# Kernel tuning notes

Hardware: AMD Instinct MI355X
Metric: run time of the kernel (lower is better)

## Reference

```python
import jax, jax.numpy as jnp
import numpy as np

N = 200000   # nodes (Elliptic-scale)
E = 500000   # directed edges
F = 166      # in_channels / node feature dim
H = 128      # hidden_channels
C = 2        # out_channels
T = 49       # number of time steps


def setup_inputs() -> dict:
    key = jax.random.key(0)
    ks = jax.random.split(key, 12)
    x = jax.random.normal(ks[0], (N, F), jnp.float32)
    edge_index = jax.random.randint(ks[1], (2, E), 0, N, dtype=jnp.int32)
    time_step = jax.random.randint(ks[2], (N,), 0, T, dtype=jnp.int32)
    sF = 1.0 / np.sqrt(F)
    sH = 1.0 / np.sqrt(H)
    initial_w = jax.random.uniform(ks[3], (F, F), jnp.float32, -sF, sF)
    gru_w_ih = jax.random.uniform(ks[4], (3 * F, F), jnp.float32, -sF, sF)
    gru_w_hh = jax.random.uniform(ks[5], (3 * F, F), jnp.float32, -sF, sF)
    gru_b_ih = jax.random.uniform(ks[6], (3 * F,), jnp.float32, -sF, sF)
    gru_b_hh = jax.random.uniform(ks[7], (3 * F,), jnp.float32, -sF, sF)
    proj_w = jax.random.uniform(ks[8], (H, F), jnp.float32, -sF, sF)
    proj_b = jax.random.uniform(ks[9], (H,), jnp.float32, -sF, sF)
    cls_w = jax.random.uniform(ks[10], (C, H), jnp.float32, -sH, sH)
    cls_b = jax.random.uniform(ks[11], (C,), jnp.float32, -sH, sH)
    return {"x": x, "edge_index": edge_index, "time_step": time_step,
            "initial_w": initial_w, "gru_w_ih": gru_w_ih, "gru_w_hh": gru_w_hh,
            "gru_b_ih": gru_b_ih, "gru_b_hh": gru_b_hh,
            "proj_w": proj_w, "proj_b": proj_b, "cls_w": cls_w, "cls_b": cls_b}


def reference(x, edge_index, time_step, initial_w, gru_w_ih, gru_w_hh,
              gru_b_ih, gru_b_hh, proj_w, proj_b, cls_w, cls_b):
    src, dst = edge_index[0], edge_index[1]
    n = x.shape[0]

    def gru(W):
        # torch.nn.GRU single step, input = hidden = W  (FxF matrix, rows = batch)
        gi = W @ gru_w_ih.T + gru_b_ih
        gh = W @ gru_w_hh.T + gru_b_hh
        i_r, i_z, i_n = jnp.split(gi, 3, axis=-1)
        h_r, h_z, h_n = jnp.split(gh, 3, axis=-1)
        r = jax.nn.sigmoid(i_r + h_r)
        z = jax.nn.sigmoid(i_z + h_z)
        nn_ = jnp.tanh(i_n + r * h_n)
        return (1.0 - z) * nn_ + z * W

    def step(carry, t):
        W, logits = carry
        W = gru(W)  # evolve GCN weight (EvolveGCN-O)
        # subgraph of nodes with time_step <= t, expressed by masking (same math
        # as relabel+extract: inactive nodes contribute nothing, their outputs are ignored)
        act = time_step <= t
        ew = (act[src] & act[dst]).astype(x.dtype)
        # gcn_norm with self-loops: deg = in-degree over active edges + 1
        deg = jax.ops.segment_sum(ew, dst, num_segments=n) + 1.0
        dinv = jax.lax.rsqrt(deg)
        norm = ew * dinv[src] * dinv[dst]
        h = jnp.where(act[:, None], x, 0.0) @ W               # [N, F]
        agg = jax.ops.segment_sum(h[src] * norm[:, None], dst, num_segments=n)
        agg = agg + h / deg[:, None]                          # self-loop term dinv_i^2 * h_i
        z = jax.nn.relu(agg @ proj_w.T + proj_b)              # [N, H] (dropout: eval mode)
        lg = z @ cls_w.T + cls_b                              # [N, C]
        logits = jnp.where((time_step == t)[:, None], lg, logits)
        return (W, logits), None

    init = (initial_w, jnp.zeros((n, cls_w.shape[0]), x.dtype))
    (_, logits), _ = jax.lax.scan(step, init, jnp.arange(T, dtype=time_step.dtype))
    return logits
```

## Files before the change

### kernel.cpp

```cpp
#include <hip/hip_runtime.h>
#include <hip/hip_fp16.h>
#include <math.h>

#define NN 200000
#define NE 500000
#define FF 166
#define HH 128
#define CC 2
#define TT 49
#define GG 498
#define PADN 203136
#define MAXTILES 6400
#define KP 84
#define KPAD 192
#define SCB 512
#define SNB 391
#define HB 782
#define CIB 1954
#define XSB 37500
#define P2B 210
#define C2B 977
#define H2B 391
#define DEGB 782
#define MBB (TT * 96)

typedef _Float16 half2v __attribute__((ext_vector_type(2)));
typedef _Float16 f16x4 __attribute__((ext_vector_type(4)));
typedef _Float16 f16x8 __attribute__((ext_vector_type(8)));
typedef float f32x4 __attribute__((ext_vector_type(4)));

static __device__ __forceinline__ float fdot2f(half2v a, half2v b, float c) {
#if __has_builtin(__builtin_amdgcn_fdot2)
    return __builtin_amdgcn_fdot2(a, b, c, false);
#else
    return c + (float)a.x * (float)b.x + (float)a.y * (float)b.y;
#endif
}

__global__ __launch_bounds__(512) void setup1(
        const float* __restrict__ wih, const float* __restrict__ whh,
        const float* __restrict__ projw,
        _Float16* __restrict__ wkp, float* __restrict__ projwT,
        const int* __restrict__ dstp, int* __restrict__ offc,
        const int* __restrict__ ts, int* __restrict__ cnt, int* __restrict__ rank) {
    __shared__ int h2[2][TT];
    int b = blockIdx.x;
    int tid = threadIdx.x;
    if (b < P2B) {
        int idx = b * 512 + tid;
        const int A = 2 * KP * 512;
        if (idx < A) {
            int m = idx / (KP * 512);
            int r = idx - m * (KP * 512);
            int kp = r >> 9, c = r & 511;
            const float* Wm = m ? whh : wih;
            float x0 = 0.0f, x1 = 0.0f;
            if (c < GG) {
                int k0 = 2 * kp, k1 = 2 * kp + 1;
                if (k0 < FF) x0 = Wm[c * FF + k0];
                if (k1 < FF) x1 = Wm[c * FF + k1];
            }
            wkp[2 * idx]     = (_Float16)x0;
            wkp[2 * idx + 1] = (_Float16)x1;
        } else if (idx < A + FF * HH) {
            int q = idx - A;
            int k = q >> 7, hh = q & 127;
            projwT[q] = projw[hh * FF + k];
        }
    } else if (b < P2B + C2B) {
        int e = (b - P2B) * 512 + tid;
        if (e < NE) atomicAdd(&offc[dstp[e]], 1);
    } else {
        int hb2 = b - P2B - C2B;
        int sub = tid >> 8;
        int lt = tid & 255;
        if (lt < TT) h2[sub][lt] = 0;
        __syncthreads();
        int i = hb2 * 512 + tid;
        if (i < NN) {
            int t = ts[i];
            rank[i] = atomicAdd(&h2[sub][t], 1);
        }
        __syncthreads();
        if (lt < TT) cnt[(hb2 * 2 + sub) * TT + lt] = h2[sub][lt];
    }
}

__global__ __launch_bounds__(512) void gru_evolve(
        const float* __restrict__ initial_w,
        const _Float16* __restrict__ wkp,
        const float* __restrict__ bih, const float* __restrict__ bhh,
        float* __restrict__ W_all) {
    __shared__ float s_w[FF];
    __shared__ __align__(16) _Float16 s_wh[2 * KP];
    __shared__ float s_pre[2][512];
    int tid = threadIdx.x;
    int row = blockIdx.x;

    if (tid < FF) {
        float v = initial_w[(size_t)row * FF + tid];
        s_w[tid] = v;
        s_wh[tid] = (_Float16)v;
    } else if (tid < 2 * KP) {
        s_wh[tid] = (_Float16)0.0f;
    }

    int cc0 = tid * 2;
    bool act = cc0 < 996;
    int m = (cc0 >= 498) ? 1 : 0;
    int c0 = act ? (cc0 - m * 498) : 0;

    half2v wr0[KP], wr1[KP];
    {
        const half2v* __restrict__ pW =
            (const half2v*)wkp + (size_t)(act ? m : 0) * (KP * 512) + c0;
        #pragma unroll
        for (int kp = 0; kp < KP; ++kp) {
            wr0[kp] = pW[(size_t)(kp << 9)];
            wr1[kp] = pW[(size_t)(kp << 9) + 1];
        }
    }

    float bi_r = 0, bi_z = 0, bi_n = 0, bh_r = 0, bh_z = 0, bh_n = 0;
    if (tid < FF) {
        bi_r = bih[tid]; bi_z = bih[FF + tid]; bi_n = bih[2 * FF + tid];
        bh_r = bhh[tid]; bh_z = bhh[FF + tid]; bh_n = bhh[2 * FF + tid];
    }
    __syncthreads();

    const f16x8* s_wh8 = (const f16x8*)s_wh;
    for (int t = 0; t < TT; ++t) {
        if (act) {
            float a0 = 0.0f, a1 = 0.0f;
            #pragma unroll
            for (int q = 0; q < 21; ++q) {
                f16x8 w8 = s_wh8[q];
                half2v h0 = __builtin_shufflevector(w8, w8, 0, 1);
                half2v h1 = __builtin_shufflevector(w8, w8, 2, 3);
                half2v h2 = __builtin_shufflevector(w8, w8, 4, 5);
                half2v h3 = __builtin_shufflevector(w8, w8, 6, 7);
                a0 = fdot2f(wr0[4 * q + 0], h0, a0);  a1 = fdot2f(wr1[4 * q + 0], h0, a1);
                a0 = fdot2f(wr0[4 * q + 1], h1, a0);  a1 = fdot2f(wr1[4 * q + 1], h1, a1);
                a0 = fdot2f(wr0[4 * q + 2], h2, a0);  a1 = fdot2f(wr1[4 * q + 2], h2, a1);
                a0 = fdot2f(wr0[4 * q + 3], h3, a0);  a1 = fdot2f(wr1[4 * q + 3], h3, a1);
            }
            s_pre[m][c0]     = a0;
            s_pre[m][c0 + 1] = a1;
        }
        __syncthreads();
        if (tid < FF) {
            float i_r = s_pre[0][tid]          + bi_r;
            float h_r = s_pre[1][tid]          + bh_r;
            float i_z = s_pre[0][FF + tid]     + bi_z;
            float h_z = s_pre[1][FF + tid]     + bh_z;
            float i_n = s_pre[0][2 * FF + tid] + bi_n;
            float h_n = s_pre[1][2 * FF + tid] + bh_n;
            float rg = 1.0f / (1.0f + expf(-(i_r + h_r)));
            float zg = 1.0f / (1.0f + expf(-(i_z + h_z)));
            float ng = tanhf(i_n + rg * h_n);
            float wnew = (1.0f - zg) * ng + zg * s_w[tid];
            s_w[tid] = wnew;
            s_wh[tid] = (_Float16)wnew;
            W_all[((size_t)t * FF + row) * FF + tid] = wnew;
        }
        __syncthreads();
    }
}

__global__ __launch_bounds__(256) void setup2(
        const int* __restrict__ off, int* __restrict__ bsum,
        const int* __restrict__ cnt, int* __restrict__ basecol, int* __restrict__ bcnt) {
    __shared__ int s[256];
    int b = blockIdx.x, tid = threadIdx.x;
    if (b < SNB) {
        int i0 = b * SCB + tid * 2;
        int v = 0;
        if (i0 < NN) v += off[i0];
        if (i0 + 1 < NN) v += off[i0 + 1];
        s[tid] = v;
        __syncthreads();
        for (int d = 128; d > 0; d >>= 1) {
            if (tid < d) s[tid] += s[tid + d];
            __syncthreads();
        }
        if (tid == 0) bsum[b] = s[0];
    } else {
        int t = b - SNB;
        const int CH = (HB + 255) / 256;
        int b0 = tid * CH;
        int loc[4];
        int sum = 0;
        for (int u = 0; u < CH; ++u) {
            int bb = b0 + u;
            int v = (bb < HB) ? cnt[bb * TT + t] : 0;
            loc[u] = sum;
            sum += v;
        }
        s[tid] = sum;
        __syncthreads();
        for (int d = 1; d < 256; d <<= 1) {
            int u = (tid >= d) ? s[tid - d] : 0;
            __syncthreads();
            s[tid] += u;
            __syncthreads();
        }
        int base = s[tid] - sum;
        for (int u = 0; u < CH; ++u) {
            int bb = b0 + u;
            if (bb < HB) basecol[bb * TT + t] = base + loc[u];
        }
        if (tid == 255) bcnt[t] = s[255];
    }
}

__global__ __launch_bounds__(512) void setup3(
        const int* __restrict__ bsum, int* __restrict__ bpre, int* __restrict__ off,
        const int* __restrict__ bcnt, int* __restrict__ pstart,
        int* __restrict__ tile_t, int* __restrict__ tile_r0, int* __restrict__ meta) {
    __shared__ int s[512];
    int tid = threadIdx.x;
    if (blockIdx.x == 0) {
        int v = (tid < SNB) ? bsum[tid] : 0;
        s[tid] = v;
        __syncthreads();
        for (int d = 1; d < 512; d <<= 1) {
            int u = (tid >= d) ? s[tid - d] : 0;
            __syncthreads();
            s[tid] += u;
            __syncthreads();
        }
        bpre[tid] = s[tid] - v;
        if (tid == 511) off[NN] = s[511];
    } else {
        int t = tid;
        int nt = (t < TT) ? (bcnt[t] + 31) / 32 : 0;
        if (t < 64) s[t] = nt;
        __syncthreads();
        for (int d = 1; d < 64; d <<= 1) {
            int v = (t >= d && t < 64) ? s[t - d] : 0;
            __syncthreads();
            if (t < 64) s[t] += v;
            __syncthreads();
        }
        if (t < 64) {
            int ntbase = s[t] - nt;
            int pbase = ntbase * 32;
            if (t < TT) {
                pstart[t] = pbase;
                for (int u = 0; u < nt; ++u) {
                    tile_t[ntbase + u] = t;
                    tile_r0[ntbase + u] = pbase + u * 32;
                }
            }
            if (t == 63) {
                meta[0] = s[63];
                meta[1] = s[63] * 32;
                pstart[TT] = s[63] * 32;
            }
        }
    }
}

__global__ __launch_bounds__(512) void setup4(
        int* __restrict__ off, const int* __restrict__ bpre,
        const int* __restrict__ ts, const int* __restrict__ rank,
        const int* __restrict__ basecol, const int* __restrict__ pstart,
        int* __restrict__ perm, int* __restrict__ pos) {
    __shared__ int s[512];
    int b = blockIdx.x, tid = threadIdx.x;
    if (b < SNB) {
        int i = b * SCB + tid;
        int v = (i < NN) ? off[i] : 0;
        s[tid] = v;
        __syncthreads();
        for (int d = 1; d < 512; d <<= 1) {
            int u = (tid >= d) ? s[tid - d] : 0;
            __syncthreads();
            s[tid] += u;
            __syncthreads();
        }
        if (i < NN) off[i] = s[tid] - v + bpre[b];
    } else {
        int i = (b - SNB) * 512 + tid;
        if (i < NN) {
            int t = ts[i];
            int hb = i >> 8;
            int p = pstart[t] + basecol[hb * TT + t] + rank[i];
            perm[p] = i;
            pos[i] = p;
        }
    }
}

__global__ __launch_bounds__(256) void setup5(
        const int* __restrict__ srcp, const int* __restrict__ dstp,
        const int* __restrict__ ts, const int* __restrict__ off,
        int* __restrict__ cursor, int2* __restrict__ adjst,
        const float* __restrict__ x, const int* __restrict__ pos,
        f16x4* __restrict__ x2p4) {
    int b = blockIdx.x, tid = threadIdx.x;
    if (b < CIB) {
        int e = b * 256 + tid;
        if (e < NE) {
            int d = dstp[e];
            int s2 = srcp[e];
            int p = atomicAdd(&cursor[d], 1);
            adjst[off[d] + p] = make_int2(s2, (ts[s2] << 25) | pos[s2]);
        }
    } else {
        int idx = (b - CIB) * 256 + tid;
        if (idx >= NN * 48) return;
        int i = idx / 48, cp4 = idx - i * 48;
        int c0 = cp4 * 4;
        float v0 = 0.f, v1 = 0.f, v2 = 0.f, v3 = 0.f;
        const float* xr = x + (size_t)i * FF;
        if (c0 + 3 < FF) {
            float2 p0 = *(const float2*)(xr + c0);
            float2 p1 = *(const float2*)(xr + c0 + 2);
            v0 = p0.x; v1 = p0.y; v2 = p1.x; v3 = p1.y;
        } else if (c0 < FF) {
            float2 p0 = *(const float2*)(xr + c0);
            v0 = p0.x; v1 = p0.y;
        }
        f16x4 h;
        h[0] = (_Float16)v0; h[1] = (_Float16)v1;
        h[2] = (_Float16)v2; h[3] = (_Float16)v3;
        x2p4[(size_t)pos[i] * 48 + cp4] = h;
    }
}

__global__ __launch_bounds__(256) void degf_m(
        const int* __restrict__ off, const int2* __restrict__ adjst,
        const int* __restrict__ ts, _Float16* __restrict__ dinvh,
        float* __restrict__ selfdeg,
        const float* __restrict__ W_all, const float* __restrict__ projwT,
        _Float16* __restrict__ Mh) {
    __shared__ unsigned short sh[TT * 256];
    __shared__ __align__(16) float sw2[2][168];
    int b = blockIdx.x;
    int tid = threadIdx.x;
    if (b < DEGB) {
        int i = b * 256 + tid;
        for (int t = 0; t < TT; ++t) sh[t * 256 + tid] = 0;
        if (i >= NN) return;
        int tsi = ts[i];
        int e0 = off[i], e1 = off[i + 1];
        for (int e = e0; e < e1; ++e) {
            int tj = adjst[e].y >> 25;
            sh[tj * 256 + tid]++;
        }
        int cum = 1;
        for (int t = 0; t < TT; ++t) {
            cum += sh[t * 256 + tid];
            dinvh[(size_t)t * NN + i] = (_Float16)rsqrtf((float)cum);
            if (t == tsi) selfdeg[i] = 1.0f / (float)cum;
        }
    } else {
        int mb = b - DEGB;
        int t = mb / 96, rb = mb - t * 96;
        int r0 = rb * 2;
        for (int idx = tid; idx < 2 * FF; idx += 256) {
            int rr = idx / FF, k = idx - rr * FF;
            int r = r0 + rr;
            sw2[rr][k] = (r < FF) ? W_all[((size_t)t * FF + r) * FF + k] : 0.0f;
        }
        __syncthreads();
        int rr = tid >> 7, h = tid & 127;
        int r = r0 + rr;
        float acc = 0.0f;
        if (r < FF) {
            const float* __restrict__ pw = projwT + h;
            #pragma unroll 4
            for (int c4 = 0; c4 < 164; c4 += 4) {
                float4 w = *(const float4*)&sw2[rr][c4];
                acc += w.x * pw[(size_t)(c4 + 0) << 7];
                acc += w.y * pw[(size_t)(c4 + 1) << 7];
                acc += w.z * pw[(size_t)(c4 + 2) << 7];
                acc += w.w * pw[(size_t)(c4 + 3) << 7];
            }
            acc += sw2[rr][164] * pw[(size_t)164 << 7];
            acc += sw2[rr][165] * pw[(size_t)165 << 7];
        }
        Mh[((size_t)t * HH + h) * KPAD + r] = (_Float16)acc;
    }
}

__global__ __launch_bounds__(256) void edge_compact(
        const int* __restrict__ off, const int2* __restrict__ adjst,
        const int* __restrict__ ts, const _Float16* __restrict__ dinvh,
        int2* __restrict__ ewp, int* __restrict__ nact) {
    int i = blockIdx.x * 256 + threadIdx.x;
    if (i >= NN) return;
    int t = ts[i];
    const _Float16* dv = dinvh + (size_t)t * NN;
    float dvi = (float)dv[i];
    int e0 = off[i], e1 = off[i + 1];
    int c = e0;
    for (int e = e0; e < e1; ++e) {
        int2 a = adjst[e];
        if ((a.y >> 25) <= t) {
            float w = (float)dv[a.x] * dvi;
            ewp[c++] = make_int2(a.y & 0x1FFFFFF, __float_as_int(w));
        }
    }
    nact[i] = c - e0;
}

__global__ __launch_bounds__(256) void gemm_fused6(
        const int* __restrict__ meta, const int* __restrict__ tile_t,
        const int* __restrict__ tile_r0, const int* __restrict__ perm,
        const float* __restrict__ selfdeg, const f16x4* __restrict__ x2p4,
        const int* __restrict__ off, const int* __restrict__ nact,
        const int2* __restrict__ ewp,
        const _Float16* __restrict__ Mh, const float* __restrict__ proj_b,
        const float* __restrict__ cls_w, const float* __restrict__ cls_b,
        float* __restrict__ out) {
    __shared__ __align__(16) char smraw[32 * 130 * 4];
    _Float16* sY = (_Float16*)smraw;
    float* sP = (float*)smraw;
    int bid = blockIdx.x;
    if (bid >= meta[0]) return;
    int t = tile_t[bid], r0 = tile_r0[bid];
    int tid = threadIdx.x;
    int lane = tid & 63;
    int w = tid >> 6;
    bool ln48 = lane < 48;

    {
        const uint4* src = (const uint4*)(x2p4 + (size_t)r0 * 48);
        #pragma unroll
        for (int u = 0; u < 3; ++u) {
            int q = tid + u * 256;
            int row = q / 24, kc = q - row * 24;
            *(uint4*)(sY + row * 200 + kc * 8) = src[q];
        }
    }
    __syncthreads();

    int rbase = w * 8;
    int ep[8], ee[8];
    float ac[8][4];
    #pragma unroll
    for (int q = 0; q < 8; ++q) {
        int r = rbase + q;
        int i = perm[r0 + r];
        float sw = 0.0f;
        ep[q] = 0; ee[q] = 0;
        if (i >= 0) {
            sw = selfdeg[i];
            ep[q] = off[i];
            ee[q] = ep[q] + nact[i];
        }
        f16x4 h = (f16x4)((_Float16)0.0f);
        if (ln48) h = *(const f16x4*)(sY + r * 200 + lane * 4);
        ac[q][0] = sw * (float)h[0];
        ac[q][1] = sw * (float)h[1];
        ac[q][2] = sw * (float)h[2];
        ac[q][3] = sw * (float)h[3];
    }
    bool more = false;
    #pragma unroll
    for (int q = 0; q < 8; ++q) more |= (ep[q] < ee[q]);
    while (more) {
        int js[8]; float wv[8];
        #pragma unroll
        for (int q = 0; q < 8; ++q) {
            bool v = ep[q] < ee[q];
            int2 p = v ? ewp[ep[q]] : make_int2(0, 0);
            js[q] = p.x;
            wv[q] = v ? __int_as_float(p.y) : 0.0f;
            if (v) ep[q]++;
        }
        #pragma unroll
        for (int q = 0; q < 8; ++q) {
            if (wv[q] != 0.0f && ln48) {
                f16x4 g = x2p4[(size_t)js[q] * 48 + lane];
                ac[q][0] += wv[q] * (float)g[0];
                ac[q][1] += wv[q] * (float)g[1];
                ac[q][2] += wv[q] * (float)g[2];
                ac[q][3] += wv[q] * (float)g[3];
            }
        }
        more = false;
        #pragma unroll
        for (int q = 0; q < 8; ++q) more |= (ep[q] < ee[q]);
    }
    #pragma unroll
    for (int q = 0; q < 8; ++q) {
        if (ln48) {
            f16x4 o;
            o[0] = (_Float16)ac[q][0];
            o[1] = (_Float16)ac[q][1];
            o[2] = (_Float16)ac[q][2];
            o[3] = (_Float16)ac[q][3];
            *(f16x4*)(sY + (rbase + q) * 200 + lane * 4) = o;
        }
    }
    __syncthreads();

    int lr = lane & 15;
    int kg = lane >> 4;
    f32x4 acc00 = {0,0,0,0}, acc01 = {0,0,0,0}, acc10 = {0,0,0,0}, acc11 = {0,0,0,0};
    const _Float16* B0 = Mh + ((size_t)t * HH + w * 32 + lr) * KPAD + kg * 8;
    const _Float16* B1 = B0 + 16 * KPAD;
    const _Float16* A0 = sY + lr * 200 + kg * 8;
    const _Float16* A1 = A0 + 16 * 200;

    #pragma unroll
    for (int s = 0; s < 6; ++s) {
        f16x8 a0 = *(const f16x8*)(A0 + s * 32);
        f16x8 a1 = *(const f16x8*)(A1 + s * 32);
        f16x8 b0 = *(const f16x8*)(B0 + s * 32);
        f16x8 b1 = *(const f16x8*)(B1 + s * 32);
        acc00 = __builtin_amdgcn_mfma_f32_16x16x32_f16(a0, b0, acc00, 0, 0, 0);
        acc01 = __builtin_amdgcn_mfma_f32_16x16x32_f16(a0, b1, acc01, 0, 0, 0);
        acc10 = __builtin_amdgcn_mfma_f32_16x16x32_f16(a1, b0, acc10, 0, 0, 0);
        acc11 = __builtin_amdgcn_mfma_f32_16x16x32_f16(a1, b1, acc11, 0, 0, 0);
    }

    float pb0 = proj_b[w * 32 + lr];
    float pb1 = proj_b[w * 32 + 16 + lr];
    __syncthreads();
    int prow = kg * 4;
    int col0 = w * 32 + lr;
    #pragma unroll
    for (int r = 0; r < 4; ++r) {
        sP[(prow + r) * 130 + col0]           = fmaxf(acc00[r] + pb0, 0.0f);
        sP[(prow + r) * 130 + col0 + 16]      = fmaxf(acc01[r] + pb1, 0.0f);
        sP[(16 + prow + r) * 130 + col0]      = fmaxf(acc10[r] + pb0, 0.0f);
        sP[(16 + prow + r) * 130 + col0 + 16] = fmaxf(acc11[r] + pb1, 0.0f);
    }
    __syncthreads();

    int row = tid >> 3, cc = (tid >> 2) & 1, qq = tid & 3;
    const float* pr = sP + row * 130 + qq * 32;
    const float* cw = cls_w + cc * HH + qq * 32;
    float s = 0.0f;
    #pragma unroll 8
    for (int h = 0; h < 32; ++h) s += pr[h] * cw[h];
    s += __shfl_xor(s, 1);
    s += __shfl_xor(s, 2);
    if (qq == 0) {
        int node = perm[r0 + row];
        if (node >= 0) out[(size_t)node * CC + cc] = s + cls_b[cc];
    }
}

extern "C" void kernel_launch(void* const* d_in, const int* in_sizes, int n_in,
                              void* d_out, int out_size, void* d_ws, size_t ws_size,
                              hipStream_t stream) {
    const float* x = (const float*)d_in[0];
    const int* ei = (const int*)d_in[1];
    const int* srcp = ei;
    const int* dstp = ei + NE;
    const int* ts = (const int*)d_in[2];
    const float* initial_w = (const float*)d_in[3];
    const float* wih = (const float*)d_in[4];
    const float* whh = (const float*)d_in[5];
    const float* bih = (const float*)d_in[6];
    const float* bhh = (const float*)d_in[7];
    const float* projw = (const float*)d_in[8];
    const float* projb = (const float*)d_in[9];
    const float* clsw = (const float*)d_in[10];
    const float* clsb = (const float*)d_in[11];
    float* out = (float*)d_out;

    char* base = (char*)d_ws;
    size_t o = 0;
    auto alloc = [&](size_t bytes) { size_t r = o; o = (o + bytes + 255) & ~(size_t)255; return r; };

    float*    W_all   = (float*)   (base + alloc((size_t)TT * FF * FF * 4));
    _Float16* Mh      = (_Float16*)(base + alloc((size_t)TT * HH * KPAD * 2));
    _Float16* wkp     = (_Float16*)(base + alloc((size_t)2 * KP * 512 * 2 * 2));
    float*    projwT  = (float*)   (base + alloc((size_t)FF * HH * 4));
    int*      off     = (int*)     (base + alloc((size_t)(NN + 1) * 4));
    int*      cursor  = (int*)     (base + alloc((size_t)NN * 4));
    int2*     adjst   = (int2*)    (base + alloc((size_t)NE * 8));
    int2*     ewp     = (int2*)    (base + alloc((size_t)NE * 8));
    _Float16* dinvh   = (_Float16*)(base + alloc((size_t)TT * NN * 2));
    float*    selfdeg = (float*)   (base + alloc((size_t)NN * 4));
    int*      nact    = (int*)     (base + alloc((size_t)NN * 4));
    int*      pos     = (int*)     (base + alloc((size_t)NN * 4));
    int*      bcnt    = (int*)     (base + alloc((size_t)TT * 4));
    int*      pstart  = (int*)     (base + alloc((size_t)(TT + 1) * 4));
    int*      meta    = (int*)     (base + alloc(2 * 4));
    int*      tile_t  = (int*)     (base + alloc((size_t)MAXTILES * 4));
    int*      tile_r0 = (int*)     (base + alloc((size_t)MAXTILES * 4));
    int*      perm    = (int*)     (base + alloc((size_t)PADN * 4));
    int*      bsum    = (int*)     (base + alloc((size_t)512 * 4));
    int*      bpre    = (int*)     (base + alloc((size_t)520 * 4));
    int*      cnt     = (int*)     (base + alloc((size_t)HB * TT * 4));
    int*      basecol = (int*)     (base + alloc((size_t)HB * TT * 4));
    int*      rank    = (int*)     (base + alloc((size_t)NN * 4));
    f16x4*    x2p4    = (f16x4*)   (base + alloc((size_t)PADN * 48 * 8));

    hipMemsetAsync(off, 0, (size_t)((char*)cursor - (char*)off) + (size_t)NN * 4, stream);
    hipMemsetAsync(perm, 0xFF, (size_t)PADN * 4, stream);

    setup1<<<P2B + C2B + H2B, 512, 0, stream>>>(wih, whh, projw, wkp, projwT,
                                                dstp, off, ts, cnt, rank);
    gru_evolve<<<FF, 512, 0, stream>>>(initial_w, wkp, bih, bhh, W_all);
    setup2<<<SNB + TT, 256, 0, stream>>>(off, bsum, cnt, basecol, bcnt);
    setup3<<<2, 512, 0, stream>>>(bsum, bpre, off, bcnt, pstart, tile_t, tile_r0, meta);
    setup4<<<SNB + SNB, 512, 0, stream>>>(off, bpre, ts, rank, basecol, pstart, perm, pos);
    setup5<<<CIB + XSB, 256, 0, stream>>>(srcp, dstp, ts, off, cursor, adjst, x, pos, x2p4);
    degf_m<<<DEGB + MBB, 256, 0, stream>>>(off, adjst, ts, dinvh, selfdeg, W_all, projwT, Mh);
    edge_compact<<<(NN + 255) / 256, 256, 0, stream>>>(off, adjst, ts, dinvh, ewp, nact);

    gemm_fused6<<<MAXTILES, 256, 0, stream>>>(meta, tile_t, tile_r0, perm, selfdeg,
                                              x2p4, off, nact, ewp, Mh, projb, clsw, clsb, out);
}
```

Measured before the change: 369.9 us.

## Use 512-thread blocks in fused gather-GEMM and prefetch next edge entries

The fused aggregation plus projection kernel now runs with 8 waves per block instead of 4. Each wave handles 4 rows of the gather instead of 8, and 16 output columns instead of 32 in the MFMA stage, and the classifier reduction is split across 8 lanes. The gather loop also loads the next edge entry from the compacted list before doing the current feature gather, which shortens the dependent-load chain. The extra waves give more latency hiding for the irregular gathers, at the cost of more threads per block and a different MFMA work split.

```diff
diff --git a/kernel.cpp b/kernel.cpp
--- a/kernel.cpp
+++ b/kernel.cpp
@@ -406,7 +406,7 @@
     nact[i] = c - e0;
 }
 
-__global__ __launch_bounds__(256) void gemm_fused6(
+__global__ __launch_bounds__(512) void gemm_fused5(
         const int* __restrict__ meta, const int* __restrict__ tile_t,
         const int* __restrict__ tile_r0, const int* __restrict__ perm,
         const float* __restrict__ selfdeg, const f16x4* __restrict__ x2p4,
@@ -429,19 +429,21 @@
     {
         const uint4* src = (const uint4*)(x2p4 + (size_t)r0 * 48);
         #pragma unroll
-        for (int u = 0; u < 3; ++u) {
-            int q = tid + u * 256;
-            int row = q / 24, kc = q - row * 24;
-            *(uint4*)(sY + row * 200 + kc * 8) = src[q];
+        for (int u = 0; u < 2; ++u) {
+            int q = tid + u * 512;
+            if (q < 768) {
+                int row = q / 24, kc = q - row * 24;
+                *(uint4*)(sY + row * 200 + kc * 8) = src[q];
+            }
         }
     }
     __syncthreads();
 
-    int rbase = w * 8;
-    int ep[8], ee[8];
-    float ac[8][4];
+    int rbase = w * 4;
+    int ep[4], ee[4];
+    float ac[4][4];
     #pragma unroll
-    for (int q = 0; q < 8; ++q) {
+    for (int q = 0; q < 4; ++q) {
         int r = rbase + q;
         int i = perm[r0 + r];
         float sw = 0.0f;
@@ -458,21 +460,22 @@
         ac[q][2] = sw * (float)h[2];
         ac[q][3] = sw * (float)h[3];
     }
-    bool more = false;
+    int2 pc[4];
     #pragma unroll
-    for (int q = 0; q < 8; ++q) more |= (ep[q] < ee[q]);
-    while (more) {
-        int js[8]; float wv[8];
+    for (int q = 0; q < 4; ++q) pc[q] = (ep[q] < ee[q]) ? ewp[ep[q]] : make_int2(0, 0);
+    while ((ep[0] < ee[0]) | (ep[1] < ee[1]) | (ep[2] < ee[2]) | (ep[3] < ee[3])) {
+        int js[4]; float wv[4];
         #pragma unroll
-        for (int q = 0; q < 8; ++q) {
-            bool v = ep[q] < ee[q];
-            int2 p = v ? ewp[ep[q]] : make_int2(0, 0);
-            js[q] = p.x;
-            wv[q] = v ? __int_as_float(p.y) : 0.0f;
-            if (v) ep[q]++;
+        for (int q = 0; q < 4; ++q) {
+            bool val = ep[q] < ee[q];
+            js[q] = pc[q].x;
+            wv[q] = val ? __int_as_float(pc[q].y) : 0.0f;
+            if (val) ep[q]++;
         }
         #pragma unroll
-        for (int q = 0; q < 8; ++q) {
+        for (int q = 0; q < 4; ++q) pc[q] = (ep[q] < ee[q]) ? ewp[ep[q]] : make_int2(0, 0);
+        #pragma unroll
+        for (int q = 0; q < 4; ++q) {
             if (wv[q] != 0.0f && ln48) {
                 f16x4 g = x2p4[(size_t)js[q] * 48 + lane];
                 ac[q][0] += wv[q] * (float)g[0];
@@ -481,12 +484,9 @@
                 ac[q][3] += wv[q] * (float)g[3];
             }
         }
-        more = false;
-        #pragma unroll
-        for (int q = 0; q < 8; ++q) more |= (ep[q] < ee[q]);
     }
     #pragma unroll
-    for (int q = 0; q < 8; ++q) {
+    for (int q = 0; q < 4; ++q) {
         if (ln48) {
             f16x4 o;
             o[0] = (_Float16)ac[q][0];
@@ -500,46 +500,41 @@
 
     int lr = lane & 15;
     int kg = lane >> 4;
-    f32x4 acc00 = {0,0,0,0}, acc01 = {0,0,0,0}, acc10 = {0,0,0,0}, acc11 = {0,0,0,0};
-    const _Float16* B0 = Mh + ((size_t)t * HH + w * 32 + lr) * KPAD + kg * 8;
-    const _Float16* B1 = B0 + 16 * KPAD;
+    int c0 = w * 16;
+    f32x4 acc0 = {0, 0, 0, 0}, acc1 = {0, 0, 0, 0};
+    const _Float16* B0 = Mh + ((size_t)t * HH + c0 + lr) * KPAD + kg * 8;
     const _Float16* A0 = sY + lr * 200 + kg * 8;
     const _Float16* A1 = A0 + 16 * 200;
 
     #pragma unroll
     for (int s = 0; s < 6; ++s) {
+        f16x8 b0 = *(const f16x8*)(B0 + s * 32);
         f16x8 a0 = *(const f16x8*)(A0 + s * 32);
         f16x8 a1 = *(const f16x8*)(A1 + s * 32);
-        f16x8 b0 = *(const f16x8*)(B0 + s * 32);
-        f16x8 b1 = *(const f16x8*)(B1 + s * 32);
-        acc00 = __builtin_amdgcn_mfma_f32_16x16x32_f16(a0, b0, acc00, 0, 0, 0);
-        acc01 = __builtin_amdgcn_mfma_f32_16x16x32_f16(a0, b1, acc01, 0, 0, 0);
-        acc10 = __builtin_amdgcn_mfma_f32_16x16x32_f16(a1, b0, acc10, 0, 0, 0);
-        acc11 = __builtin_amdgcn_mfma_f32_16x16x32_f16(a1, b1, acc11, 0, 0, 0);
-    }
-
-    float pb0 = proj_b[w * 32 + lr];
-    float pb1 = proj_b[w * 32 + 16 + lr];
+        acc0 = __builtin_amdgcn_mfma_f32_16x16x32_f16(a0, b0, acc0, 0, 0, 0);
+        acc1 = __builtin_amdgcn_mfma_f32_16x16x32_f16(a1, b0, acc1, 0, 0, 0);
+    }
+
+    float pb = proj_b[c0 + lr];
     __syncthreads();
     int prow = kg * 4;
-    int col0 = w * 32 + lr;
+    int colw = c0 + lr;
     #pragma unroll
     for (int r = 0; r < 4; ++r) {
-        sP[(prow + r) * 130 + col0]           = fmaxf(acc00[r] + pb0, 0.0f);
-        sP[(prow + r) * 130 + col0 + 16]      = fmaxf(acc01[r] + pb1, 0.0f);
-        sP[(16 + prow + r) * 130 + col0]      = fmaxf(acc10[r] + pb0, 0.0f);
-        sP[(16 + prow + r) * 130 + col0 + 16] = fmaxf(acc11[r] + pb1, 0.0f);
+        sP[(prow + r) * 130 + colw]      = fmaxf(acc0[r] + pb, 0.0f);
+        sP[(16 + prow + r) * 130 + colw] = fmaxf(acc1[r] + pb, 0.0f);
     }
     __syncthreads();
 
-    int row = tid >> 3, cc = (tid >> 2) & 1, qq = tid & 3;
-    const float* pr = sP + row * 130 + qq * 32;
-    const float* cw = cls_w + cc * HH + qq * 32;
+    int row = tid >> 4, cc = (tid >> 3) & 1, qq = tid & 7;
+    const float* pr = sP + row * 130 + qq * 16;
+    const float* cw = cls_w + cc * HH + qq * 16;
     float s = 0.0f;
-    #pragma unroll 8
-    for (int h = 0; h < 32; ++h) s += pr[h] * cw[h];
+    #pragma unroll
+    for (int h = 0; h < 16; ++h) s += pr[h] * cw[h];
     s += __shfl_xor(s, 1);
     s += __shfl_xor(s, 2);
+    s += __shfl_xor(s, 4);
     if (qq == 0) {
         int node = perm[r0 + row];
         if (node >= 0) out[(size_t)node * CC + cc] = s + cls_b[cc];
@@ -607,6 +602,6 @@
     degf_m<<<DEGB + MBB, 256, 0, stream>>>(off, adjst, ts, dinvh, selfdeg, W_all, projwT, Mh);
     edge_compact<<<(NN + 255) / 256, 256, 0, stream>>>(off, adjst, ts, dinvh, ewp, nact);
 
-    gemm_fused6<<<MAXTILES, 256, 0, stream>>>(meta, tile_t, tile_r0, perm, selfdeg,
+    gemm_fused5<<<MAXTILES, 512, 0, stream>>>(meta, tile_t, tile_r0, perm, selfdeg,
                                               x2p4, off, nact, ewp, Mh, projb, clsw, clsb, out);
 }
```

Result: faster. 326.0 us (-11.9%).
